# Performance work log

Hardware: AMD Instinct MI355X
Metric: run time of the kernel (lower is better)

Reference implementation:

```python
import jax, jax.numpy as jnp
import numpy as np

B, T, D_MODEL = 2, 2048, 2048
N_HEAD, N_KV, HD = 32, 8, 64


def _rope_tables(T, hd, base=10000.0):
    # standard rotary tables, (T, hd) with frequencies repeated over both halves
    inv_freq = 1.0 / (base ** (np.arange(0, hd // 2, dtype=np.float32) / (hd // 2)))
    t = np.arange(T, dtype=np.float32)
    freqs = np.outer(t, inv_freq)            # (T, hd/2)
    emb = np.concatenate([freqs, freqs], axis=-1)  # (T, hd)
    return jnp.asarray(np.cos(emb)), jnp.asarray(np.sin(emb))


def setup_inputs() -> dict:
    key = jax.random.key(0)
    ks = jax.random.split(key, 5)
    cos, sin = _rope_tables(T, HD)
    s = 0.02
    return {
        "x": jax.random.normal(ks[0], (B, T, D_MODEL), jnp.float32),
        "cos": cos,
        "sin": sin,
        "Wq": jax.random.normal(ks[1], (N_HEAD * HD, D_MODEL), jnp.float32) * s,
        "Wk": jax.random.normal(ks[2], (N_KV * HD, D_MODEL), jnp.float32) * s,
        "Wv": jax.random.normal(ks[3], (N_KV * HD, D_MODEL), jnp.float32) * s,
        "Wo": jax.random.normal(ks[4], (D_MODEL, N_HEAD * HD), jnp.float32) * s,
    }


def _apply_rope(x, cos, sin):
    # x: (B, H, T, D); cos/sin: (T, D)
    D = x.shape[-1]
    x1, x2 = x[..., : D // 2], x[..., D // 2 :]
    rot = jnp.concatenate([-x2, x1], axis=-1)
    c = cos[: x.shape[-2]][None, None]
    s = sin[: x.shape[-2]][None, None]
    return x * c + rot * s


def reference(x, cos, sin, Wq, Wk, Wv, Wo):
    Bv, Tv, _ = x.shape
    q = (x @ Wq.T).reshape(Bv, Tv, N_HEAD, HD).transpose(0, 2, 1, 3)  # (B,H,T,D)
    k = (x @ Wk.T).reshape(Bv, Tv, N_KV, HD).transpose(0, 2, 1, 3)    # (B,Hkv,T,D)
    v = (x @ Wv.T).reshape(Bv, Tv, N_KV, HD).transpose(0, 2, 1, 3)
    q = _apply_rope(q, cos, sin)
    k = _apply_rope(k, cos, sin)
    repeat = N_HEAD // N_KV
    if repeat > 1:
        k = jnp.repeat(k, repeat, axis=1)
        v = jnp.repeat(v, repeat, axis=1)
    scale = 1.0 / jnp.sqrt(jnp.float32(HD)).astype(x.dtype)
    scores = jnp.einsum("bhqd,bhkd->bhqk", q, k) * scale
    causal = jnp.tril(jnp.ones((Tv, Tv), dtype=bool))
    scores = jnp.where(causal[None, None], scores, jnp.finfo(scores.dtype).min)
    attn = jax.nn.softmax(scores, axis=-1)
    out = jnp.einsum("bhqk,bhkd->bhqd", attn, v)
    out = out.transpose(0, 2, 1, 3).reshape(Bv, Tv, N_HEAD * HD)
    return out @ Wo.T
```

## Files before the change

kernel.cpp:

```cpp
#include <hip/hip_runtime.h>
#include <stdint.h>

#define B_SZ 2
#define T_SEQ 2048
#define DM 2048
#define NH 32
#define NKV 8
#define HD 64
#define QKV_W 3072

typedef unsigned short u16;
typedef __bf16 bf16x8 __attribute__((ext_vector_type(8)));
typedef float floatx4 __attribute__((ext_vector_type(4)));

__device__ __forceinline__ float bf2f(u16 u) {
  union { unsigned u; float f; } v; v.u = ((unsigned)u) << 16; return v.f;
}
__device__ __forceinline__ u16 f2bf(float f) {
  union { float f; unsigned u; } v; v.f = f;
  unsigned r = v.u + 0x7fff + ((v.u >> 16) & 1);
  return (u16)(r >> 16);
}
__device__ __forceinline__ unsigned pk2bf(float hi, float lo) {
  return __builtin_amdgcn_perm(__float_as_uint(hi), __float_as_uint(lo), 0x07060302u);
}
__device__ __forceinline__ float fexp2(float x) {
#if __has_builtin(__builtin_amdgcn_exp2f)
  return __builtin_amdgcn_exp2f(x);
#else
  return exp2f(x);
#endif
}

__device__ __forceinline__ void gld_lds16(const void* g, void* l) {
  __builtin_amdgcn_global_load_lds(
      (const __attribute__((address_space(1))) unsigned int*)g,
      (__attribute__((address_space(3))) unsigned int*)l, 16, 0, 0);
}

__global__ __launch_bounds__(256) void conv_kernel(
    const float* __restrict__ src, u16* __restrict__ dst, int n4)
{
  int i = blockIdx.x * 256 + threadIdx.x;
  int stride = gridDim.x * 256;
  for (; i < n4; i += stride) {
    float4 v = ((const float4*)src)[i];
    ushort4 o;
    o.x = f2bf(v.x); o.y = f2bf(v.y); o.z = f2bf(v.z); o.w = f2bf(v.w);
    ((ushort4*)dst)[i] = o;
  }
}

__global__ __launch_bounds__(256) void gemm_qkv_kernel(
    const u16* __restrict__ A, const u16* __restrict__ Bt,
    u16* __restrict__ C)
{
  __shared__ __align__(16) u16 sA[128 * 32];
  __shared__ __align__(16) u16 sB[128 * 32];

  const int n0 = blockIdx.x * 128;
  const int m0 = blockIdx.y * 128;
  const int K = 2048;

  const int tid  = threadIdx.x;
  const int lane = tid & 63;
  const int w    = tid >> 6;
  const int wm = w >> 1, wn = w & 1;
  const int lm = lane & 15, lq = lane >> 4;

  floatx4 acc[4][4];
  #pragma unroll
  for (int i = 0; i < 4; i++)
    #pragma unroll
    for (int j = 0; j < 4; j++) { floatx4 z = {0.f,0.f,0.f,0.f}; acc[i][j] = z; }

  const int ar = tid >> 2;
  const int ac = (tid & 3) * 8;
  const u16* Ap0 = A  + (size_t)(m0 + ar) * K + ac;
  const u16* Ap1 = A  + (size_t)(m0 + 64 + ar) * K + ac;
  const u16* Bp0 = Bt + (size_t)(n0 + ar) * K + ac;
  const u16* Bp1 = Bt + (size_t)(n0 + 64 + ar) * K + ac;
  u16* sAd = sA + tid * 8;
  u16* sBd = sB + tid * 8;

  for (int k0 = 0; k0 < K; k0 += 32) {
    gld_lds16(Ap0 + k0, sAd);
    gld_lds16(Ap1 + k0, sAd + 2048);
    gld_lds16(Bp0 + k0, sBd);
    gld_lds16(Bp1 + k0, sBd + 2048);
    __syncthreads();

    bf16x8 af[4], bfr[4];
    #pragma unroll
    for (int mi = 0; mi < 4; mi++)
      af[mi] = *(const bf16x8*)(sA + (wm*64 + mi*16 + lm)*32 + lq*8);
    #pragma unroll
    for (int ni = 0; ni < 4; ni++)
      bfr[ni] = *(const bf16x8*)(sB + (wn*64 + ni*16 + lm)*32 + lq*8);

    #pragma unroll
    for (int mi = 0; mi < 4; mi++)
      #pragma unroll
      for (int ni = 0; ni < 4; ni++)
        acc[mi][ni] = __builtin_amdgcn_mfma_f32_16x16x32_bf16(
            af[mi], bfr[ni], acc[mi][ni], 0, 0, 0);
    __syncthreads();
  }

  #pragma unroll
  for (int mi = 0; mi < 4; mi++)
    #pragma unroll
    for (int ni = 0; ni < 4; ni++)
      #pragma unroll
      for (int r = 0; r < 4; r++) {
        int row = m0 + wm*64 + mi*16 + lq*4 + r;
        int col = n0 + wn*64 + ni*16 + lm;
        C[(size_t)row * QKV_W + col] = f2bf(acc[mi][ni][r]);
      }
}

__global__ __launch_bounds__(256) void gemm_out_kernel(
    const u16* __restrict__ A, const u16* __restrict__ Bt,
    float* __restrict__ C)
{
  __shared__ __align__(16) u16 sA[128 * 32];
  __shared__ __align__(16) u16 sB[128 * 32];

  const int n0 = blockIdx.x * 128;
  const int m0 = blockIdx.y * 128;
  const int K = 2048;

  const int tid  = threadIdx.x;
  const int lane = tid & 63;
  const int w    = tid >> 6;
  const int wm = w >> 1, wn = w & 1;
  const int lm = lane & 15, lq = lane >> 4;

  floatx4 acc[4][4];
  #pragma unroll
  for (int i = 0; i < 4; i++)
    #pragma unroll
    for (int j = 0; j < 4; j++) { floatx4 z = {0.f,0.f,0.f,0.f}; acc[i][j] = z; }

  const int ar = tid >> 2;
  const int ac = (tid & 3) * 8;
  const u16* Ap0 = A  + (size_t)(m0 + ar) * K + ac;
  const u16* Ap1 = A  + (size_t)(m0 + 64 + ar) * K + ac;
  const u16* Bp0 = Bt + (size_t)(n0 + ar) * K + ac;
  const u16* Bp1 = Bt + (size_t)(n0 + 64 + ar) * K + ac;
  u16* sAd = sA + tid * 8;
  u16* sBd = sB + tid * 8;

  for (int k0 = 0; k0 < K; k0 += 32) {
    gld_lds16(Ap0 + k0, sAd);
    gld_lds16(Ap1 + k0, sAd + 2048);
    gld_lds16(Bp0 + k0, sBd);
    gld_lds16(Bp1 + k0, sBd + 2048);
    __syncthreads();

    bf16x8 af[4], bfr[4];
    #pragma unroll
    for (int mi = 0; mi < 4; mi++)
      af[mi] = *(const bf16x8*)(sA + (wm*64 + mi*16 + lm)*32 + lq*8);
    #pragma unroll
    for (int ni = 0; ni < 4; ni++)
      bfr[ni] = *(const bf16x8*)(sB + (wn*64 + ni*16 + lm)*32 + lq*8);

    #pragma unroll
    for (int mi = 0; mi < 4; mi++)
      #pragma unroll
      for (int ni = 0; ni < 4; ni++)
        acc[mi][ni] = __builtin_amdgcn_mfma_f32_16x16x32_bf16(
            af[mi], bfr[ni], acc[mi][ni], 0, 0, 0);
    __syncthreads();
  }

  #pragma unroll
  for (int mi = 0; mi < 4; mi++)
    #pragma unroll
    for (int ni = 0; ni < 4; ni++)
      #pragma unroll
      for (int r = 0; r < 4; r++) {
        int row = m0 + wm*64 + mi*16 + lq*4 + r;
        int col = n0 + wn*64 + ni*16 + lm;
        C[(size_t)row * DM + col] = acc[mi][ni][r];
      }
}

#define QSCALE 0.180336880f
__global__ __launch_bounds__(256) void rope_kernel(
    const u16* __restrict__ qkv, const float* __restrict__ cosf,
    const float* __restrict__ sinf, u16* __restrict__ qb, u16* __restrict__ kb)
{
  const int bt = blockIdx.x;
  const int b = bt / T_SEQ, t = bt % T_SEQ;
  const int tid = threadIdx.x;
  const u16* row = qkv + (size_t)bt * QKV_W;

  #pragma unroll
  for (int i = 0; i < 4; i++) {
    int idx = i * 256 + tid;
    int h = idx >> 5, dp = idx & 31;
    float x1 = bf2f(row[h * 64 + dp]);
    float x2 = bf2f(row[h * 64 + dp + 32]);
    float c = cosf[t * 64 + dp];
    float s = sinf[t * 64 + dp];
    float o1 = (x1 * c - x2 * s) * QSCALE;
    float o2 = (x2 * c + x1 * s) * QSCALE;
    size_t base = ((size_t)(b * NH + h) * T_SEQ + t) * HD + dp;
    qb[base]      = f2bf(o1);
    qb[base + 32] = f2bf(o2);
  }
  {
    int idx = tid;
    int kvh = idx >> 5, dp = idx & 31;
    float x1 = bf2f(row[2048 + kvh * 64 + dp]);
    float x2 = bf2f(row[2048 + kvh * 64 + dp + 32]);
    float c = cosf[t * 64 + dp];
    float s = sinf[t * 64 + dp];
    size_t base = ((size_t)(b * NKV + kvh) * T_SEQ + t) * HD + dp;
    kb[base]      = f2bf(x1 * c - x2 * s);
    kb[base + 32] = f2bf(x2 * c + x1 * s);
  }
}

__global__ __launch_bounds__(256) void vtrans_kernel(
    const u16* __restrict__ qkv, u16* __restrict__ vbt)
{
  __shared__ u16 tile[64][66];
  const int t0  = blockIdx.x * 64;
  const int kvh = blockIdx.y;
  const int b   = blockIdx.z;
  const int tid = threadIdx.x;

  #pragma unroll
  for (int i = 0; i < 16; i++) {
    int idx = i * 256 + tid;
    int r = idx >> 6, c = idx & 63;
    tile[r][c] = qkv[(size_t)(b * T_SEQ + t0 + r) * QKV_W + 2560 + kvh * 64 + c];
  }
  __syncthreads();
  #pragma unroll
  for (int i = 0; i < 16; i++) {
    int idx = i * 256 + tid;
    int d = idx >> 6, c = idx & 63;
    vbt[((size_t)(b * NKV + kvh) * HD + d) * T_SEQ + t0 + c] = tile[c][d];
  }
}

__global__ __launch_bounds__(256, 2) void attn_kernel(
    const u16* __restrict__ qb, const u16* __restrict__ kb,
    const u16* __restrict__ vbt, u16* __restrict__ attn)
{
  __shared__ __align__(16) u16 sK[64 * 64];
  __shared__ __align__(16) u16 sV[64 * 64];
  __shared__ __align__(16) u16 sP[4][16][72];
  __shared__ float sAl[4][16];

  const int tid  = threadIdx.x;
  const int lane = tid & 63;
  const int w    = tid >> 6;

  const int l  = blockIdx.x;
  const int qt = 63 - (l >> 4);
  const int kv = l & 7;
  const int b  = (l >> 3) & 1;
  const int h  = kv * 4 + w;
  const int ktmax = qt >> 1;
  const int moff  = 32 * (qt & 1);

  const int lm = lane & 15, lq = lane >> 4;
  const int sw = lm & 7;

  bf16x8 qf[2][2];
  {
    const u16* qhead = qb + ((size_t)(b * NH + h) * T_SEQ + qt * 32) * HD;
    #pragma unroll
    for (int nq = 0; nq < 2; nq++) {
      const u16* qrow = qhead + (size_t)(nq * 16 + lm) * HD + lq * 8;
      qf[nq][0] = *(const bf16x8*)(qrow);
      qf[nq][1] = *(const bf16x8*)(qrow + 32);
    }
  }

  floatx4 o_acc[2][4];
  #pragma unroll
  for (int i = 0; i < 2; i++)
    #pragma unroll
    for (int j = 0; j < 4; j++) { floatx4 z = {0.f,0.f,0.f,0.f}; o_acc[i][j] = z; }
  float m_run[2] = {-1e30f, -1e30f};
  float l_run[2] = {0.f, 0.f};

  const u16* kbase = kb  + (size_t)(b * NKV + kv) * T_SEQ * HD;
  const u16* vbase = vbt + (size_t)(b * NKV + kv) * HD * T_SEQ;

  const int p0row = tid >> 3,        p1row = (256 + tid) >> 3;
  const int p0ck  = (tid & 7) ^ (p0row & 7), p1ck = ((256 + tid) & 7) ^ (p1row & 7);
  const u16* kp0 = kbase + (size_t)p0row * HD + p0ck * 8;
  const u16* kp1 = kbase + (size_t)p1row * HD + p1ck * 8;
  const u16* vp0 = vbase + (size_t)p0row * T_SEQ + p0ck * 8;
  const u16* vp1 = vbase + (size_t)p1row * T_SEQ + p1ck * 8;
  char* sKd0 = (char*)sK + tid * 16;        char* sKd1 = (char*)sK + (256 + tid) * 16;
  char* sVd0 = (char*)sV + tid * 16;        char* sVd1 = (char*)sV + (256 + tid) * 16;

  for (int kt = 0; kt <= ktmax; kt++) {
    __syncthreads();
    gld_lds16(kp0 + (size_t)kt * 64 * HD, sKd0);
    gld_lds16(kp1 + (size_t)kt * 64 * HD, sKd1);
    gld_lds16(vp0 + kt * 64, sVd0);
    gld_lds16(vp1 + kt * 64, sVd1);
    __syncthreads();

    bf16x8 kf[4][2], vf[4][2];
    #pragma unroll
    for (int nt = 0; nt < 4; nt++) {
      kf[nt][0] = *(const bf16x8*)(sK + (((nt*16 + lm) * 8 + (lq ^ sw)) << 3));
      kf[nt][1] = *(const bf16x8*)(sK + (((nt*16 + lm) * 8 + ((4 + lq) ^ sw)) << 3));
      vf[nt][0] = *(const bf16x8*)(sV + (((nt*16 + lm) * 8 + (lq ^ sw)) << 3));
      vf[nt][1] = *(const bf16x8*)(sV + (((nt*16 + lm) * 8 + ((4 + lq) ^ sw)) << 3));
    }

    #pragma unroll
    for (int nq = 0; nq < 2; nq++) {
      floatx4 s_acc[4];
      #pragma unroll
      for (int nt = 0; nt < 4; nt++) {
        floatx4 z = {0.f,0.f,0.f,0.f};
        z = __builtin_amdgcn_mfma_f32_16x16x32_bf16(kf[nt][0], qf[nq][0], z, 0, 0, 0);
        z = __builtin_amdgcn_mfma_f32_16x16x32_bf16(kf[nt][1], qf[nq][1], z, 0, 0, 0);
        s_acc[nt] = z;
      }

      if (kt == ktmax) {
        #pragma unroll
        for (int nt = 0; nt < 4; nt++)
          #pragma unroll
          for (int r = 0; r < 4; r++)
            if (nt * 16 + lq * 4 + r > nq * 16 + lm + moff) s_acc[nt][r] = -1e30f;
      }

      float mloc = s_acc[0][0];
      #pragma unroll
      for (int nt = 0; nt < 4; nt++)
        #pragma unroll
        for (int r = 0; r < 4; r++) mloc = fmaxf(mloc, s_acc[nt][r]);
      mloc = fmaxf(mloc, __shfl_xor(mloc, 16));
      mloc = fmaxf(mloc, __shfl_xor(mloc, 32));
      float mnew = fmaxf(m_run[nq], mloc);
      float al = fexp2(m_run[nq] - mnew);

      float rs = 0.f;
      uint2 pk[4];
      #pragma unroll
      for (int nt = 0; nt < 4; nt++) {
        float p0 = fexp2(s_acc[nt][0] - mnew);
        float p1 = fexp2(s_acc[nt][1] - mnew);
        float p2 = fexp2(s_acc[nt][2] - mnew);
        float p3 = fexp2(s_acc[nt][3] - mnew);
        rs += (p0 + p1) + (p2 + p3);
        pk[nt].x = pk2bf(p1, p0);
        pk[nt].y = pk2bf(p3, p2);
      }
      rs += __shfl_xor(rs, 16);
      rs += __shfl_xor(rs, 32);
      l_run[nq] = l_run[nq] * al + rs;
      m_run[nq] = mnew;

      #pragma unroll
      for (int nt = 0; nt < 4; nt++)
        *(uint2*)&sP[w][lm][nt * 16 + lq * 4] = pk[nt];

      if (lq == 0) sAl[w][lm] = al;
      floatx4 alv = *(const floatx4*)&sAl[w][lq * 4];
      #pragma unroll
      for (int nd = 0; nd < 4; nd++)
        #pragma unroll
        for (int r = 0; r < 4; r++)
          o_acc[nq][nd][r] *= alv[r];

      #pragma unroll
      for (int st = 0; st < 2; st++) {
        bf16x8 pf = *(const bf16x8*)(&sP[w][lm][st * 32 + lq * 8]);
        #pragma unroll
        for (int nd = 0; nd < 4; nd++)
          o_acc[nq][nd] = __builtin_amdgcn_mfma_f32_16x16x32_bf16(
              pf, vf[nd][st], o_acc[nq][nd], 0, 0, 0);
      }
    }
  }

  #pragma unroll
  for (int nq = 0; nq < 2; nq++) {
    __builtin_amdgcn_s_waitcnt(0);
    if (lq == 0) sAl[w][lm] = l_run[nq];
    floatx4 lv = *(const floatx4*)&sAl[w][lq * 4];
    #pragma unroll
    for (int nd = 0; nd < 4; nd++)
      #pragma unroll
      for (int r = 0; r < 4; r++) {
        float v = o_acc[nq][nd][r] / lv[r];
        size_t row = (size_t)b * T_SEQ + qt * 32 + nq * 16 + lq * 4 + r;
        attn[row * DM + h * HD + nd * 16 + lm] = f2bf(v);
      }
  }
}

extern "C" void kernel_launch(void* const* d_in, const int* in_sizes, int n_in,
                              void* d_out, int out_size, void* d_ws, size_t ws_size,
                              hipStream_t stream)
{
  const float* x    = (const float*)d_in[0];
  const float* cosf = (const float*)d_in[1];
  const float* sinf = (const float*)d_in[2];
  const float* Wq   = (const float*)d_in[3];
  const float* Wk   = (const float*)d_in[4];
  const float* Wv   = (const float*)d_in[5];
  const float* Wo   = (const float*)d_in[6];
  float* out = (float*)d_out;

  char* ws = (char*)d_ws;
  u16* qkvb  = (u16*)(ws + 0);
  u16* attnb = (u16*)(ws + 0);
  u16* qb    = (u16*)(ws + 25165824);
  u16* kb    = (u16*)(ws + 41943040);
  u16* vbt   = (u16*)(ws + 46137344);
  u16* xb    = (u16*)(ws + 50331648);
  u16* wob   = (u16*)(ws + 50331648);
  u16* wqkvb = (u16*)(ws + 67108864);

  dim3 blk(256);
  conv_kernel<<<dim3(2048), blk, 0, stream>>>(x,  xb,                 8388608 / 4);
  conv_kernel<<<dim3(1024), blk, 0, stream>>>(Wq, wqkvb,              4194304 / 4);
  conv_kernel<<<dim3(512),  blk, 0, stream>>>(Wk, wqkvb + 2048*2048,  1048576 / 4);
  conv_kernel<<<dim3(512),  blk, 0, stream>>>(Wv, wqkvb + 2560*2048,  1048576 / 4);

  gemm_qkv_kernel<<<dim3(24, 32), blk, 0, stream>>>(xb, wqkvb, qkvb);

  conv_kernel<<<dim3(1024), blk, 0, stream>>>(Wo, wob, 4194304 / 4);

  rope_kernel<<<dim3(B_SZ * T_SEQ), blk, 0, stream>>>(qkvb, cosf, sinf, qb, kb);
  vtrans_kernel<<<dim3(T_SEQ / 64, NKV, B_SZ), blk, 0, stream>>>(qkvb, vbt);
  attn_kernel<<<dim3(1024), blk, 0, stream>>>(qb, kb, vbt, attnb);
  gemm_out_kernel<<<dim3(16, 32), blk, 0, stream>>>(attnb, wob, out);
}
```

Baseline: 317.5 us.

## Merge weight conversions, skip small max rescales, raise MFMA priority and occupancy

Fuses the three QKV weight fp32-to-bf16 conversions into one launch to cut launch overhead. In attention, the online-softmax rescale of the output accumulator is skipped unless the running max rises by more than 8 (log2 domain) for some lane, which removes a shared-memory round trip and multiplies on most tiles. It also wraps the MFMA blocks in s_setprio and raises launch bounds to 3 blocks per CU. The lazy rescale stays exact but lets exponentials grow up to 2^8, which risks bf16 precision loss in P. The higher occupancy bound may also cause register spills.

```diff
diff --git a/kernel.cpp b/kernel.cpp
--- a/kernel.cpp
+++ b/kernel.cpp
@@ -45,6 +45,23 @@
   int stride = gridDim.x * 256;
   for (; i < n4; i += stride) {
     float4 v = ((const float4*)src)[i];
+    ushort4 o;
+    o.x = f2bf(v.x); o.y = f2bf(v.y); o.z = f2bf(v.z); o.w = f2bf(v.w);
+    ((ushort4*)dst)[i] = o;
+  }
+}
+
+__global__ __launch_bounds__(256) void conv_wqkv_kernel(
+    const float* __restrict__ Wq, const float* __restrict__ Wk,
+    const float* __restrict__ Wv, u16* __restrict__ dst)
+{
+  int i = blockIdx.x * 256 + threadIdx.x;
+  int stride = gridDim.x * 256;
+  for (; i < 1572864; i += stride) {
+    float4 v;
+    if (i < 1048576)      v = ((const float4*)Wq)[i];
+    else if (i < 1310720) v = ((const float4*)Wk)[i - 1048576];
+    else                  v = ((const float4*)Wv)[i - 1310720];
     ushort4 o;
     o.x = f2bf(v.x); o.y = f2bf(v.y); o.z = f2bf(v.z); o.w = f2bf(v.w);
     ((ushort4*)dst)[i] = o;
@@ -248,7 +265,7 @@
   }
 }
 
-__global__ __launch_bounds__(256, 2) void attn_kernel(
+__global__ __launch_bounds__(256, 3) void attn_kernel(
     const u16* __restrict__ qb, const u16* __restrict__ kb,
     const u16* __restrict__ vbt, u16* __restrict__ attn)
 {
@@ -323,6 +340,7 @@
     #pragma unroll
     for (int nq = 0; nq < 2; nq++) {
       floatx4 s_acc[4];
+      __builtin_amdgcn_s_setprio(1);
       #pragma unroll
       for (int nt = 0; nt < 4; nt++) {
         floatx4 z = {0.f,0.f,0.f,0.f};
@@ -330,6 +348,7 @@
         z = __builtin_amdgcn_mfma_f32_16x16x32_bf16(kf[nt][1], qf[nq][1], z, 0, 0, 0);
         s_acc[nt] = z;
       }
+      __builtin_amdgcn_s_setprio(0);
 
       if (kt == ktmax) {
         #pragma unroll
@@ -346,8 +365,21 @@
         for (int r = 0; r < 4; r++) mloc = fmaxf(mloc, s_acc[nt][r]);
       mloc = fmaxf(mloc, __shfl_xor(mloc, 16));
       mloc = fmaxf(mloc, __shfl_xor(mloc, 32));
-      float mnew = fmaxf(m_run[nq], mloc);
-      float al = fexp2(m_run[nq] - mnew);
+
+      float mnew = m_run[nq];
+      if (!__all(mloc - m_run[nq] <= 8.0f)) {
+        mnew = fmaxf(m_run[nq], mloc);
+        float al = fexp2(m_run[nq] - mnew);
+        m_run[nq] = mnew;
+        l_run[nq] *= al;
+        if (lq == 0) sAl[w][lm] = al;
+        floatx4 alv = *(const floatx4*)&sAl[w][lq * 4];
+        #pragma unroll
+        for (int nd = 0; nd < 4; nd++)
+          #pragma unroll
+          for (int r = 0; r < 4; r++)
+            o_acc[nq][nd][r] *= alv[r];
+      }
 
       float rs = 0.f;
       uint2 pk[4];
@@ -363,21 +395,13 @@
       }
       rs += __shfl_xor(rs, 16);
       rs += __shfl_xor(rs, 32);
-      l_run[nq] = l_run[nq] * al + rs;
-      m_run[nq] = mnew;
+      l_run[nq] += rs;
 
       #pragma unroll
       for (int nt = 0; nt < 4; nt++)
         *(uint2*)&sP[w][lm][nt * 16 + lq * 4] = pk[nt];
 
-      if (lq == 0) sAl[w][lm] = al;
-      floatx4 alv = *(const floatx4*)&sAl[w][lq * 4];
-      #pragma unroll
-      for (int nd = 0; nd < 4; nd++)
-        #pragma unroll
-        for (int r = 0; r < 4; r++)
-          o_acc[nq][nd][r] *= alv[r];
-
+      __builtin_amdgcn_s_setprio(1);
       #pragma unroll
       for (int st = 0; st < 2; st++) {
         bf16x8 pf = *(const bf16x8*)(&sP[w][lm][st * 32 + lq * 8]);
@@ -386,6 +410,7 @@
           o_acc[nq][nd] = __builtin_amdgcn_mfma_f32_16x16x32_bf16(
               pf, vf[nd][st], o_acc[nq][nd], 0, 0, 0);
       }
+      __builtin_amdgcn_s_setprio(0);
     }
   }
 
@@ -429,10 +454,8 @@
   u16* wqkvb = (u16*)(ws + 67108864);
 
   dim3 blk(256);
-  conv_kernel<<<dim3(2048), blk, 0, stream>>>(x,  xb,                 8388608 / 4);
-  conv_kernel<<<dim3(1024), blk, 0, stream>>>(Wq, wqkvb,              4194304 / 4);
-  conv_kernel<<<dim3(512),  blk, 0, stream>>>(Wk, wqkvb + 2048*2048,  1048576 / 4);
-  conv_kernel<<<dim3(512),  blk, 0, stream>>>(Wv, wqkvb + 2560*2048,  1048576 / 4);
+  conv_kernel<<<dim3(2048), blk, 0, stream>>>(x, xb, 8388608 / 4);
+  conv_wqkv_kernel<<<dim3(1536), blk, 0, stream>>>(Wq, Wk, Wv, wqkvb);
 
   gemm_qkv_kernel<<<dim3(24, 32), blk, 0, stream>>>(xb, wqkvb, qkvb);
 
```

Result: no change. 317.9 us (+0.1%).
